# Performance work log

Hardware: AMD Instinct MI355X
Metric: run time of the kernel (lower is better)

## Reference

```python
import jax, jax.numpy as jnp
import numpy as np

B, S, D = 4, 1024, 1024
L, H, DK, DV, DFF = 2, 8, 128, 128, 2048
MASK_VALUE = -1e-30
LN_EPS = 1e-14  # K.epsilon()**2 with K.epsilon()=1e-7


def _glorot(key, shape):
    fan_in, fan_out = shape[-2], shape[-1]
    lim = np.sqrt(6.0 / (fan_in + fan_out)).astype(np.float32)
    return jax.random.uniform(key, shape, jnp.float32, -lim, lim)


def setup_inputs() -> dict:
    key = jax.random.key(0)
    ks = jax.random.split(key, 8)
    return {
        "x": jax.random.normal(ks[0], (B, S, D), jnp.float32),
        "mask": jnp.ones((B, S), jnp.float32),
        "Wq": _glorot(ks[1], (L, H, D, DK)),
        "Wk": _glorot(ks[2], (L, H, D, DK)),
        "Wv": _glorot(ks[3], (L, H, D, DV)),
        "Wo": _glorot(ks[4], (L, H * DV, D)),
        "W1": _glorot(ks[5], (L, D, DFF)),
        "b1": jnp.zeros((L, DFF), jnp.float32),
        "W2": _glorot(ks[6], (L, DFF, D)),
        "b2": jnp.zeros((L, D), jnp.float32),
        "gamma": jnp.ones((2 * L,), jnp.float32),
        "beta": jnp.zeros((2 * L,), jnp.float32),
    }


def _layernorm(x, g, b):
    mean = jnp.mean(x, axis=-1, keepdims=True)
    var = jnp.mean(jnp.square(x - mean), axis=-1, keepdims=True)
    return (x - mean) / jnp.sqrt(var + LN_EPS) * g + b


def reference(x, mask, Wq, Wk, Wv, Wo, W1, b1, W2, b2, gamma, beta):
    m = mask[:, None, None, :]  # [B,1,1,S] broadcast over heads and query positions
    num_layers = Wq.shape[0]
    for i in range(num_layers):
        # All heads at once (faithful to the per-head loop: identical math)
        q = jnp.einsum("bsd,hdk->bhsk", x, Wq[i])
        k = jnp.einsum("bsd,hdk->bhsk", x, Wk[i])
        v = jnp.einsum("bsd,hdv->bhsv", x, Wv[i])
        A = jnp.einsum("bhsk,bhtk->bhst", q, k)  # NOTE: no 1/sqrt(dk) scaling in original
        A = m * A + (1.0 - m) * MASK_VALUE
        A = jax.nn.softmax(A, axis=-1)
        o = jnp.einsum("bhst,bhtv->bhsv", A, v)
        conc = o.transpose(0, 2, 1, 3).reshape(x.shape[0], x.shape[1], -1)  # [B,S,H*DV]
        proj = conc @ Wo[i]
        x = _layernorm(x + proj, gamma[2 * i], beta[2 * i])
        ffn = jax.nn.relu(x @ W1[i] + b1[i]) @ W2[i] + b2[i]
        x = _layernorm(x + ffn, gamma[2 * i + 1], beta[2 * i + 1])
    return x
```

## Files before the change

### kernel.cpp

```cpp
#include <hip/hip_runtime.h>
#include <hip/hip_bf16.h>


typedef __bf16 bf16_t;
typedef bf16_t bf16x8 __attribute__((ext_vector_type(8)));
typedef bf16_t bf16x4v __attribute__((ext_vector_type(4)));
typedef float f32x4 __attribute__((ext_vector_type(4)));

#define MFMA16(a, b, c) __builtin_amdgcn_mfma_f32_16x16x32_bf16((a), (b), (c), 0, 0, 0)

__device__ __align__(256) unsigned char g_ws[(size_t)192 << 20];

#define MBOFF(x) ((size_t)(x) << 20)
#define OFF_X32 MBOFF(0)
#define OFF_XB_HI MBOFF(16)
#define OFF_XB_LO MBOFF(24)
#define OFF_QKV_HI MBOFF(32)
#define OFF_QKV_LO MBOFF(56)
#define OFF_VT_HI MBOFF(80)
#define OFF_VT_LO MBOFF(88)
#define OFF_CONC_HI MBOFF(96)
#define OFF_CONC_LO MBOFF(104)
#define OFF_TMP MBOFF(112)
#define OFF_H_HI MBOFF(128)
#define OFF_H_LO MBOFF(144)
#define OFF_WQKV_HI MBOFF(160)
#define OFF_WQKV_LO MBOFF(166)
#define OFF_WO_HI MBOFF(172)
#define OFF_WO_LO MBOFF(174)
#define OFF_W1_HI MBOFF(176)
#define OFF_W1_LO MBOFF(180)
#define OFF_W2_HI MBOFF(184)
#define OFF_W2_LO MBOFF(188)
#define OFF_TMP2 MBOFF(32)

__device__ __forceinline__ void split2(float v, bf16_t& h, bf16_t& l) {
  h = (bf16_t)v;
  l = (bf16_t)(v - (float)h);
}

__device__ __forceinline__ void gl2lds16(const bf16_t* g, bf16_t* l) {
  __builtin_amdgcn_global_load_lds(
      (const __attribute__((address_space(1))) unsigned int*)(g),
      (__attribute__((address_space(3))) unsigned int*)(l), 16, 0, 0);
}

template <int EPI>
__global__ __launch_bounds__(512) void gemm_bt(
    size_t a_hi, size_t a_lo, size_t b_hi, size_t b_lo,
    size_t c0o, size_t c1o, const float* __restrict__ bias,
    int M, int N, int Ktot, int Ksl) {
  const bf16_t* Ah = (const bf16_t*)(g_ws + a_hi);
  const bf16_t* Al = (const bf16_t*)(g_ws + a_lo);
  const bf16_t* Bh = (const bf16_t*)(g_ws + b_hi);
  const bf16_t* Bl = (const bf16_t*)(g_ws + b_lo);
  __shared__ __align__(16) bf16_t Ash[128 * 32];
  __shared__ __align__(16) bf16_t Asl[128 * 32];
  __shared__ __align__(16) bf16_t Bsh[128 * 32];
  __shared__ __align__(16) bf16_t Bsl[128 * 32];
  const int tid = threadIdx.x;
  const int wave = tid >> 6, lane = tid & 63;
  const int quad = lane >> 4, l16 = lane & 15;
  const int wm = wave & 3, wn = wave >> 2;
  const int m0 = blockIdx.y * 128, n0 = blockIdx.x * 128;
  const int z = blockIdx.z;
  const int srow = wave * 16 + (lane >> 2);
  const int scp = (lane & 3) ^ ((srow >> 1) & 3);
  const long agoff = (long)(m0 + srow) * Ktot + (long)z * Ksl + scp * 8;
  const long bgoff = (long)(n0 + srow) * Ktot + (long)z * Ksl + scp * 8;
  bf16_t* ldsA = Ash + wave * 512;
  bf16_t* ldsAl = Asl + wave * 512;
  bf16_t* ldsB = Bsh + wave * 512;
  bf16_t* ldsBl = Bsl + wave * 512;
  int aOff[2], bOff[4];
#pragma unroll
  for (int mt = 0; mt < 2; ++mt) {
    int R = wm * 32 + mt * 16 + l16;
    aOff[mt] = R * 32 + ((quad ^ ((R >> 1) & 3)) * 8);
  }
#pragma unroll
  for (int nt = 0; nt < 4; ++nt) {
    int R = wn * 64 + nt * 16 + l16;
    bOff[nt] = R * 32 + ((quad ^ ((R >> 1) & 3)) * 8);
  }
  f32x4 acc[2][4] = {};

  for (int k0 = 0; k0 < Ksl; k0 += 32) {
    gl2lds16(Ah + agoff + k0, ldsA);
    gl2lds16(Al + agoff + k0, ldsAl);
    gl2lds16(Bh + bgoff + k0, ldsB);
    gl2lds16(Bl + bgoff + k0, ldsBl);
    __syncthreads();
    bf16x8 ah[2], al[2], bhf[4], blf[4];
#pragma unroll
    for (int mt = 0; mt < 2; ++mt) {
      ah[mt] = *(const bf16x8*)(Ash + aOff[mt]);
      al[mt] = *(const bf16x8*)(Asl + aOff[mt]);
    }
#pragma unroll
    for (int nt = 0; nt < 4; ++nt) {
      bhf[nt] = *(const bf16x8*)(Bsh + bOff[nt]);
      blf[nt] = *(const bf16x8*)(Bsl + bOff[nt]);
    }
#pragma unroll
    for (int mt = 0; mt < 2; ++mt)
#pragma unroll
      for (int nt = 0; nt < 4; ++nt) {
        acc[mt][nt] = MFMA16(ah[mt], bhf[nt], acc[mt][nt]);
        acc[mt][nt] = MFMA16(ah[mt], blf[nt], acc[mt][nt]);
        acc[mt][nt] = MFMA16(al[mt], bhf[nt], acc[mt][nt]);
      }
    __syncthreads();
  }

  float* Cf = (float*)(g_ws + (z == 0 ? c0o : c1o));
  bf16_t* Ch = (bf16_t*)(g_ws + c0o);
  bf16_t* Cl = (bf16_t*)(g_ws + c1o);
#pragma unroll
  for (int mt = 0; mt < 2; ++mt) {
    const int row0 = m0 + wm * 32 + mt * 16 + quad * 4;
#pragma unroll
    for (int nt = 0; nt < 4; ++nt) {
      const int col = n0 + wn * 64 + nt * 16 + l16;
      float bv = ((EPI >= 2) && z == 0) ? bias[col] : 0.0f;
#pragma unroll
      for (int r = 0; r < 4; ++r) {
        float v = acc[mt][nt][r] + bv;
        if (EPI == 2) v = fmaxf(v, 0.0f);
        long off = (long)(row0 + r) * N + col;
        if (EPI == 0 || EPI == 3) {
          Cf[off] = v;
        } else {
          bf16_t h, l;
          split2(v, h, l);
          Ch[off] = h;
          Cl[off] = l;
        }
      }
    }
  }
}

__global__ __launch_bounds__(256) void attn_kernel(const float* __restrict__ mask) {
  const bf16_t* QKVh = (const bf16_t*)(g_ws + OFF_QKV_HI);
  const bf16_t* QKVl = (const bf16_t*)(g_ws + OFF_QKV_LO);
  const bf16_t* VTh = (const bf16_t*)(g_ws + OFF_VT_HI);
  const bf16_t* VTl = (const bf16_t*)(g_ws + OFF_VT_LO);
  bf16_t* conch = (bf16_t*)(g_ws + OFF_CONC_HI);
  bf16_t* concl = (bf16_t*)(g_ws + OFF_CONC_LO);
  __shared__ __align__(16) bf16_t Ksh[64 * 128];
  __shared__ __align__(16) bf16_t Ksl[64 * 128];
  __shared__ __align__(16) bf16_t Vsh[128 * 64];
  __shared__ __align__(16) bf16_t Vsl[128 * 64];
  __shared__ __align__(16) bf16_t Ps[4][16 * 72];
  const int tid = threadIdx.x;
  const int wave = tid >> 6, lane = tid & 63;
  const int quad = lane >> 4, l16 = lane & 15;
  const int q0 = blockIdx.x * 64;
  const int bh = blockIdx.y, b = bh >> 3, h = bh & 7;

  bf16x8 qfh[4], qfl[4];
  const long qgbase = ((long)(b * 1024) + q0 + wave * 16 + l16) * 3072 + h * 128;
#pragma unroll
  for (int ks = 0; ks < 4; ++ks) {
    qfh[ks] = *(const bf16x8*)(QKVh + qgbase + ks * 32 + quad * 8);
    qfl[ks] = *(const bf16x8*)(QKVl + qgbase + ks * 32 + quad * 8);
  }

  const int sKrow4 = wave * 16 + (lane >> 4);
  const int sVrow = wave * 32 + (lane >> 3);
  const int sVc = (lane & 7) ^ (sVrow & 7);
  const long vgbase = (long)bh * 131072 + (long)sVrow * 1024 + sVc * 8;

  f32x4 o[8] = {};
  float mi[4] = {-1e30f, -1e30f, -1e30f, -1e30f};
  float li[4] = {0.f, 0.f, 0.f, 0.f};

  for (int t0 = 0; t0 < 1024; t0 += 64) {
#pragma unroll
    for (int j = 0; j < 4; ++j) {
      const int r = sKrow4 + j * 4;
      const int c = (lane & 15) ^ ((r & 7) * 2);
      const long kg = ((long)(b * 1024) + t0 + r) * 3072 + 1024 + h * 128 + c * 8;
      gl2lds16(QKVh + kg, Ksh + (wave * 16 + j * 4) * 128);
      gl2lds16(QKVl + kg, Ksl + (wave * 16 + j * 4) * 128);
    }
#pragma unroll
    for (int j = 0; j < 4; ++j) {
      const long vg = vgbase + (long)(j * 8) * 1024 + t0;
      gl2lds16(VTh + vg, Vsh + (wave * 32 + j * 8) * 64);
      gl2lds16(VTl + vg, Vsl + (wave * 32 + j * 8) * 64);
    }
    __syncthreads();
    f32x4 s4[4] = {};
#pragma unroll
    for (int nt = 0; nt < 4; ++nt) {
      const int krow = nt * 16 + l16;
      const int ksw = (krow & 7) * 2;
#pragma unroll
      for (int ks = 0; ks < 4; ++ks) {
        const int so = krow * 128 + (((ks * 4 + quad) ^ ksw) * 8);
        bf16x8 kfh = *(const bf16x8*)(Ksh + so);
        bf16x8 kfl = *(const bf16x8*)(Ksl + so);
        s4[nt] = MFMA16(qfh[ks], kfh, s4[nt]);
        s4[nt] = MFMA16(qfh[ks], kfl, s4[nt]);
        s4[nt] = MFMA16(qfl[ks], kfh, s4[nt]);
      }
    }
#pragma unroll
    for (int nt = 0; nt < 4; ++nt) {
      float mv = mask[b * 1024 + t0 + nt * 16 + l16];
      float addv = (1.0f - mv) * (-1e-30f);
#pragma unroll
      for (int r = 0; r < 4; ++r) s4[nt][r] = mv * s4[nt][r] + addv;
    }
#pragma unroll
    for (int r = 0; r < 4; ++r) {
      float mx = fmaxf(fmaxf(s4[0][r], s4[1][r]), fmaxf(s4[2][r], s4[3][r]));
#pragma unroll
      for (int off = 1; off < 16; off <<= 1) mx = fmaxf(mx, __shfl_xor(mx, off, 64));
      float mnew = fmaxf(mi[r], mx);
      float alpha = __expf(mi[r] - mnew);
      float rs = 0.0f;
#pragma unroll
      for (int nt = 0; nt < 4; ++nt) {
        float p = __expf(s4[nt][r] - mnew);
        s4[nt][r] = p;
        rs += p;
      }
#pragma unroll
      for (int off = 1; off < 16; off <<= 1) rs += __shfl_xor(rs, off, 64);
      li[r] = li[r] * alpha + rs;
      mi[r] = mnew;
#pragma unroll
      for (int on = 0; on < 8; ++on) o[on][r] *= alpha;
    }
#pragma unroll
    for (int nt = 0; nt < 4; ++nt)
#pragma unroll
      for (int r = 0; r < 4; ++r)
        Ps[wave][(quad * 4 + r) * 72 + nt * 16 + l16] = (bf16_t)s4[nt][r];
    bf16x8 pf[2];
#pragma unroll
    for (int k2 = 0; k2 < 2; ++k2)
      pf[k2] = *(const bf16x8*)(&Ps[wave][l16 * 72 + k2 * 32 + quad * 8]);
#pragma unroll
    for (int k2 = 0; k2 < 2; ++k2) {
#pragma unroll
      for (int on = 0; on < 8; ++on) {
        const int vrow = on * 16 + l16;
        const int so = vrow * 64 + (((k2 * 4 + quad) ^ (vrow & 7)) * 8);
        bf16x8 vfh = *(const bf16x8*)(Vsh + so);
        bf16x8 vfl = *(const bf16x8*)(Vsl + so);
        o[on] = MFMA16(pf[k2], vfh, o[on]);
        o[on] = MFMA16(pf[k2], vfl, o[on]);
      }
    }
    __syncthreads();
  }
  const int srow_o = q0 + wave * 16 + quad * 4;
#pragma unroll
  for (int r = 0; r < 4; ++r) {
    float inv = 1.0f / li[r];
#pragma unroll
    for (int on = 0; on < 8; ++on) {
      float v = o[on][r] * inv;
      bf16_t hh, ll;
      split2(v, hh, ll);
      long off = (long)(b * 1024 + srow_o + r) * 1024 + h * 128 + on * 16 + l16;
      conch[off] = hh;
      concl[off] = ll;
    }
  }
}

__global__ __launch_bounds__(256) void ln_kernel(
    const float* __restrict__ gamma, const float* __restrict__ beta, int gidx,
    float* __restrict__ extf) {
  const float* xres = (const float*)(g_ws + OFF_X32);
  const float* y1 = (const float*)(g_ws + OFF_TMP);
  const float* y2 = (const float*)(g_ws + OFF_TMP2);
  float* xout = (float*)(g_ws + OFF_X32);
  bf16_t* xbh = (bf16_t*)(g_ws + OFF_XB_HI);
  bf16_t* xbl = (bf16_t*)(g_ws + OFF_XB_LO);
  const int row = blockIdx.x, tid = threadIdx.x;
  const int wave = tid >> 6, lane = tid & 63;
  const long base = (long)row * 1024 + tid * 4;
  float4 xv = *(const float4*)(xres + base);
  float4 yv = *(const float4*)(y1 + base);
  float4 y2v = *(const float4*)(y2 + base);
  float v0 = xv.x + yv.x + y2v.x, v1 = xv.y + yv.y + y2v.y;
  float v2 = xv.z + yv.z + y2v.z, v3 = xv.w + yv.w + y2v.w;
  float s1 = v0 + v1 + v2 + v3;
  float s2 = v0 * v0 + v1 * v1 + v2 * v2 + v3 * v3;
#pragma unroll
  for (int off = 1; off < 64; off <<= 1) {
    s1 += __shfl_xor(s1, off, 64);
    s2 += __shfl_xor(s2, off, 64);
  }
  __shared__ __align__(16) float r1[4], r2[4];
  if (lane == 0) { r1[wave] = s1; r2[wave] = s2; }
  __syncthreads();
  s1 = r1[0] + r1[1] + r1[2] + r1[3];
  s2 = r2[0] + r2[1] + r2[2] + r2[3];
  const float mean = s1 * (1.0f / 1024.0f);
  float var = s2 * (1.0f / 1024.0f) - mean * mean;
  var = fmaxf(var, 0.0f);
  const float inv = rsqrtf(var + 1e-14f);
  const float g = gamma[gidx], be = beta[gidx];
  float o0 = (v0 - mean) * inv * g + be;
  float o1 = (v1 - mean) * inv * g + be;
  float o2 = (v2 - mean) * inv * g + be;
  float o3 = (v3 - mean) * inv * g + be;
  float4 ov = {o0, o1, o2, o3};
  *(float4*)(xout + base) = ov;
  if (extf) {
    *(float4*)(extf + base) = ov;
  } else {
    bf16_t h0, l0, h1, l1, h2, l2, h3, l3;
    split2(o0, h0, l0); split2(o1, h1, l1);
    split2(o2, h2, l2); split2(o3, h3, l3);
    bf16x4v hv = {h0, h1, h2, h3};
    bf16x4v lv = {l0, l1, l2, l3};
    *(bf16x4v*)(xbh + base) = hv;
    *(bf16x4v*)(xbl + base) = lv;
  }
}

__global__ __launch_bounds__(256) void cast_f2b(const float* __restrict__ in) {
  float* out = (float*)(g_ws + OFF_X32);
  bf16_t* outh = (bf16_t*)(g_ws + OFF_XB_HI);
  bf16_t* outl = (bf16_t*)(g_ws + OFF_XB_LO);
  long i = ((long)blockIdx.x * 256 + threadIdx.x) * 4;
  float4 v = *(const float4*)(in + i);
  *(float4*)(out + i) = v;
  bf16_t h0, l0, h1, l1, h2, l2, h3, l3;
  split2(v.x, h0, l0); split2(v.y, h1, l1);
  split2(v.z, h2, l2); split2(v.w, h3, l3);
  bf16x4v hv = {h0, h1, h2, h3};
  bf16x4v lv = {l0, l1, l2, l3};
  *(bf16x4v*)(outh + i) = hv;
  *(bf16x4v*)(outl + i) = lv;
}

__global__ __launch_bounds__(256) void transp_split(
    const float* __restrict__ in, size_t oh_off, size_t ol_off, int R, int C) {
  bf16_t* oh = (bf16_t*)(g_ws + oh_off);
  bf16_t* ol = (bf16_t*)(g_ws + ol_off);
  __shared__ float tile[32][33];
  const int tx = threadIdx.x, ty = threadIdx.y;
  const int c0 = blockIdx.x * 32, r0 = blockIdx.y * 32;
#pragma unroll
  for (int j = 0; j < 4; ++j)
    tile[ty + j * 8][tx] = in[(long)(r0 + ty + j * 8) * C + c0 + tx];
  __syncthreads();
#pragma unroll
  for (int j = 0; j < 4; ++j) {
    float v = tile[tx][ty + j * 8];
    bf16_t h, l;
    split2(v, h, l);
    long off = (long)(c0 + ty + j * 8) * R + r0 + tx;
    oh[off] = h;
    ol[off] = l;
  }
}

__global__ __launch_bounds__(256) void qkvw_trans(
    const float* __restrict__ Wq, const float* __restrict__ Wk,
    const float* __restrict__ Wv) {
  bf16_t* oh = (bf16_t*)(g_ws + OFF_WQKV_HI);
  bf16_t* ol = (bf16_t*)(g_ws + OFF_WQKV_LO);
  __shared__ float tile[32][33];
  const int tx = threadIdx.x, ty = threadIdx.y;
  const int z = blockIdx.z, mat = z >> 3, h = z & 7;
  const float* src = (mat == 0 ? Wq : (mat == 1 ? Wk : Wv)) + h * 131072;
  const int c0 = blockIdx.x * 32, r0 = blockIdx.y * 32;
#pragma unroll
  for (int j = 0; j < 4; ++j)
    tile[ty + j * 8][tx] = src[(r0 + ty + j * 8) * 128 + c0 + tx];
  __syncthreads();
  const int nbase = mat * 1024 + h * 128;
#pragma unroll
  for (int j = 0; j < 4; ++j) {
    float v = tile[tx][ty + j * 8];
    bf16_t hh, ll;
    split2(v, hh, ll);
    long off = (long)(nbase + c0 + ty + j * 8) * 1024 + r0 + tx;
    oh[off] = hh;
    ol[off] = ll;
  }
}

__global__ __launch_bounds__(256) void vt_trans() {
  const bf16_t* QKVh = (const bf16_t*)(g_ws + OFF_QKV_HI);
  const bf16_t* QKVl = (const bf16_t*)(g_ws + OFF_QKV_LO);
  bf16_t* VTh = (bf16_t*)(g_ws + OFF_VT_HI);
  bf16_t* VTl = (bf16_t*)(g_ws + OFF_VT_LO);
  __shared__ bf16_t th[32][34];
  __shared__ bf16_t tl[32][34];
  const int tx = threadIdx.x, ty = threadIdx.y;
  const int bh = blockIdx.z, b = bh >> 3, h = bh & 7;
  const int s0 = blockIdx.x * 32, v0 = blockIdx.y * 32;
#pragma unroll
  for (int j = 0; j < 4; ++j) {
    long src = ((long)(b * 1024) + s0 + ty + j * 8) * 3072 + 2048 + h * 128 + v0 + tx;
    th[ty + j * 8][tx] = QKVh[src];
    tl[ty + j * 8][tx] = QKVl[src];
  }
  __syncthreads();
#pragma unroll
  for (int j = 0; j < 4; ++j) {
    long off = (long)bh * 131072 + (long)(v0 + ty + j * 8) * 1024 + s0 + tx;
    VTh[off] = th[tx][ty + j * 8];
    VTl[off] = tl[tx][ty + j * 8];
  }
}

extern "C" void kernel_launch(void* const* d_in, const int* in_sizes, int n_in,
                              void* d_out, int out_size, void* d_ws, size_t ws_size,
                              hipStream_t stream) {
  const float* x_in = (const float*)d_in[0];
  const float* mask = (const float*)d_in[1];
  const float* Wq = (const float*)d_in[2];
  const float* Wk = (const float*)d_in[3];
  const float* Wv = (const float*)d_in[4];
  const float* Wo = (const float*)d_in[5];
  const float* W1 = (const float*)d_in[6];
  const float* b1 = (const float*)d_in[7];
  const float* W2 = (const float*)d_in[8];
  const float* b2 = (const float*)d_in[9];
  const float* gamma = (const float*)d_in[10];
  const float* beta = (const float*)d_in[11];
  float* out = (float*)d_out;
  (void)d_ws; (void)ws_size; (void)in_sizes; (void)n_in; (void)out_size;

  const dim3 tb(32, 8);
  cast_f2b<<<4096, 256, 0, stream>>>(x_in);

  for (int l = 0; l < 2; ++l) {
    qkvw_trans<<<dim3(4, 32, 24), tb, 0, stream>>>(
        Wq + (long)l * 1048576, Wk + (long)l * 1048576, Wv + (long)l * 1048576);
    transp_split<<<dim3(32, 32), tb, 0, stream>>>(Wo + (long)l * 1048576,
                                                  OFF_WO_HI, OFF_WO_LO, 1024, 1024);
    transp_split<<<dim3(64, 32), tb, 0, stream>>>(W1 + (long)l * 2097152,
                                                  OFF_W1_HI, OFF_W1_LO, 1024, 2048);
    transp_split<<<dim3(32, 64), tb, 0, stream>>>(W2 + (long)l * 2097152,
                                                  OFF_W2_HI, OFF_W2_LO, 2048, 1024);

    gemm_bt<1><<<dim3(24, 32, 1), 512, 0, stream>>>(
        OFF_XB_HI, OFF_XB_LO, OFF_WQKV_HI, OFF_WQKV_LO,
        OFF_QKV_HI, OFF_QKV_LO, nullptr, 4096, 3072, 1024, 1024);
    vt_trans<<<dim3(32, 4, 32), tb, 0, stream>>>();
    attn_kernel<<<dim3(16, 32), 256, 0, stream>>>(mask);
    gemm_bt<0><<<dim3(8, 32, 2), 512, 0, stream>>>(
        OFF_CONC_HI, OFF_CONC_LO, OFF_WO_HI, OFF_WO_LO,
        OFF_TMP, OFF_TMP2, nullptr, 4096, 1024, 1024, 512);
    ln_kernel<<<4096, 256, 0, stream>>>(gamma, beta, 2 * l, nullptr);
    gemm_bt<2><<<dim3(16, 32, 1), 512, 0, stream>>>(
        OFF_XB_HI, OFF_XB_LO, OFF_W1_HI, OFF_W1_LO,
        OFF_H_HI, OFF_H_LO, b1 + l * 2048, 4096, 2048, 1024, 1024);
    gemm_bt<3><<<dim3(8, 32, 2), 512, 0, stream>>>(
        OFF_H_HI, OFF_H_LO, OFF_W2_HI, OFF_W2_LO,
        OFF_TMP, OFF_TMP2, b2 + l * 1024, 4096, 1024, 2048, 1024);
    ln_kernel<<<4096, 256, 0, stream>>>(gamma, beta, 2 * l + 1,
                                        (l == 1) ? out : nullptr);
  }
}
```

Baseline: 835.1 us.

## Add 256x256-tile double-buffered split-bf16 GEMM for QKV projection

```diff
diff --git a/kernel.cpp b/kernel.cpp
--- a/kernel.cpp
+++ b/kernel.cpp
@@ -43,6 +43,150 @@
   __builtin_amdgcn_global_load_lds(
       (const __attribute__((address_space(1))) unsigned int*)(g),
       (__attribute__((address_space(3))) unsigned int*)(l), 16, 0, 0);
+}
+
+template <int EPI>
+__global__ __launch_bounds__(512, 2) void gemm256(
+    size_t a_hi, size_t a_lo, size_t b_hi, size_t b_lo,
+    size_t c0o, size_t c1o, const float* __restrict__ bias,
+    int M, int N, int Ktot, int Ksl) {
+  const bf16_t* Ah = (const bf16_t*)(g_ws + a_hi);
+  const bf16_t* Al = (const bf16_t*)(g_ws + a_lo);
+  const bf16_t* Bh = (const bf16_t*)(g_ws + b_hi);
+  const bf16_t* Bl = (const bf16_t*)(g_ws + b_lo);
+  __shared__ __align__(16) bf16_t sAh[2][256 * 32];
+  __shared__ __align__(16) bf16_t sAl[2][256 * 32];
+  __shared__ __align__(16) bf16_t sBh[2][256 * 32];
+  __shared__ __align__(16) bf16_t sBl[2][256 * 32];
+  const int tid = threadIdx.x;
+  const int wave = tid >> 6, lane = tid & 63;
+  const int quad = lane >> 4, l16 = lane & 15;
+  const int wm = wave & 1, wn = wave >> 1;
+  const int m0 = blockIdx.y * 256, n0 = blockIdx.x * 256;
+  const int srow_s = lane >> 2;
+  const int scp = (lane & 3) ^ ((lane >> 3) & 3);
+  const long aoff0 = (long)(m0 + wave * 32 + srow_s) * Ktot + scp * 8;
+  const long aoff1 = aoff0 + (long)16 * Ktot;
+  const long boff0 = (long)(n0 + wave * 32 + srow_s) * Ktot + scp * 8;
+  const long boff1 = boff0 + (long)16 * Ktot;
+  const int ldsw0 = wave * 1024;
+  const int ldsw1 = wave * 1024 + 512;
+  const int fsw = quad ^ ((l16 >> 1) & 3);
+  int aOff[8], bOff[4];
+#pragma unroll
+  for (int mt = 0; mt < 8; ++mt)
+    aOff[mt] = (wm * 128 + mt * 16 + l16) * 32 + fsw * 8;
+#pragma unroll
+  for (int nt = 0; nt < 4; ++nt)
+    bOff[nt] = (wn * 64 + nt * 16 + l16) * 32 + fsw * 8;
+
+  f32x4 acc[8][4] = {};
+  const int nk = Ksl >> 5;
+
+#define STAGE_H1(bufi, ko)                      \
+  gl2lds16(Ah + aoff0 + (ko), &sAh[bufi][ldsw0]); \
+  gl2lds16(Al + aoff0 + (ko), &sAl[bufi][ldsw0]); \
+  gl2lds16(Bh + boff0 + (ko), &sBh[bufi][ldsw0]); \
+  gl2lds16(Bl + boff0 + (ko), &sBl[bufi][ldsw0]);
+#define STAGE_H2(bufi, ko)                      \
+  gl2lds16(Ah + aoff1 + (ko), &sAh[bufi][ldsw1]); \
+  gl2lds16(Al + aoff1 + (ko), &sAl[bufi][ldsw1]); \
+  gl2lds16(Bh + boff1 + (ko), &sBh[bufi][ldsw1]); \
+  gl2lds16(Bl + boff1 + (ko), &sBl[bufi][ldsw1]);
+
+  STAGE_H1(0, 0);
+  STAGE_H2(0, 0);
+
+  for (int t = 0; t < nk; ++t) {
+    const int cur = t & 1, nxt = cur ^ 1;
+    const int ko = (t + 1) * 32;
+    const bool pf = (t + 1 < nk);
+    if (pf) {
+      STAGE_H1(nxt, ko);
+      asm volatile("s_waitcnt vmcnt(4)" ::: "memory");
+    } else {
+      asm volatile("s_waitcnt vmcnt(0)" ::: "memory");
+    }
+    __builtin_amdgcn_sched_barrier(0);
+    __builtin_amdgcn_s_barrier();
+    __builtin_amdgcn_sched_barrier(0);
+    bf16x8 bh4[4], bl4[4], ah2[4], al2[4];
+#pragma unroll
+    for (int nt = 0; nt < 4; ++nt) {
+      bh4[nt] = *(const bf16x8*)(&sBh[cur][bOff[nt]]);
+      bl4[nt] = *(const bf16x8*)(&sBl[cur][bOff[nt]]);
+    }
+#pragma unroll
+    for (int mt = 0; mt < 4; ++mt) {
+      ah2[mt] = *(const bf16x8*)(&sAh[cur][aOff[mt]]);
+      al2[mt] = *(const bf16x8*)(&sAl[cur][aOff[mt]]);
+    }
+    asm volatile("s_waitcnt lgkmcnt(0)" ::: "memory");
+    __builtin_amdgcn_sched_barrier(0);
+    __builtin_amdgcn_s_setprio(1);
+#pragma unroll
+    for (int mt = 0; mt < 4; ++mt)
+#pragma unroll
+      for (int nt = 0; nt < 4; ++nt) {
+        acc[mt][nt] = MFMA16(ah2[mt], bh4[nt], acc[mt][nt]);
+        acc[mt][nt] = MFMA16(ah2[mt], bl4[nt], acc[mt][nt]);
+        acc[mt][nt] = MFMA16(al2[mt], bh4[nt], acc[mt][nt]);
+      }
+    __builtin_amdgcn_s_setprio(0);
+    __builtin_amdgcn_sched_barrier(0);
+    __builtin_amdgcn_s_barrier();
+    if (pf) {
+      STAGE_H2(nxt, ko);
+    }
+#pragma unroll
+    for (int mt = 0; mt < 4; ++mt) {
+      ah2[mt] = *(const bf16x8*)(&sAh[cur][aOff[mt + 4]]);
+      al2[mt] = *(const bf16x8*)(&sAl[cur][aOff[mt + 4]]);
+    }
+    asm volatile("s_waitcnt lgkmcnt(0)" ::: "memory");
+    __builtin_amdgcn_sched_barrier(0);
+    __builtin_amdgcn_s_setprio(1);
+#pragma unroll
+    for (int mt = 0; mt < 4; ++mt)
+#pragma unroll
+      for (int nt = 0; nt < 4; ++nt) {
+        acc[mt + 4][nt] = MFMA16(ah2[mt], bh4[nt], acc[mt + 4][nt]);
+        acc[mt + 4][nt] = MFMA16(ah2[mt], bl4[nt], acc[mt + 4][nt]);
+        acc[mt + 4][nt] = MFMA16(al2[mt], bh4[nt], acc[mt + 4][nt]);
+      }
+    __builtin_amdgcn_s_setprio(0);
+    __builtin_amdgcn_sched_barrier(0);
+    __builtin_amdgcn_s_barrier();
+  }
+#undef STAGE_H1
+#undef STAGE_H2
+
+  float* Cf = (float*)(g_ws + c0o);
+  bf16_t* Ch = (bf16_t*)(g_ws + c0o);
+  bf16_t* Cl = (bf16_t*)(g_ws + c1o);
+#pragma unroll
+  for (int mt = 0; mt < 8; ++mt) {
+    const int row0 = m0 + wm * 128 + mt * 16 + quad * 4;
+#pragma unroll
+    for (int nt = 0; nt < 4; ++nt) {
+      const int col = n0 + wn * 64 + nt * 16 + l16;
+      float bv = (EPI >= 2) ? bias[col] : 0.0f;
+#pragma unroll
+      for (int r = 0; r < 4; ++r) {
+        float v = acc[mt][nt][r] + bv;
+        if (EPI == 2) v = fmaxf(v, 0.0f);
+        long off = (long)(row0 + r) * N + col;
+        if (EPI == 0 || EPI == 3) {
+          Cf[off] = v;
+        } else {
+          bf16_t h, l;
+          split2(v, h, l);
+          Ch[off] = h;
+          Cl[off] = l;
+        }
+      }
+    }
+  }
 }
 
 template <int EPI>
@@ -447,7 +591,7 @@
     transp_split<<<dim3(32, 64), tb, 0, stream>>>(W2 + (long)l * 2097152,
                                                   OFF_W2_HI, OFF_W2_LO, 2048, 1024);
 
-    gemm_bt<1><<<dim3(24, 32, 1), 512, 0, stream>>>(
+    gemm256<1><<<dim3(12, 16, 1), 512, 0, stream>>>(
         OFF_XB_HI, OFF_XB_LO, OFF_WQKV_HI, OFF_WQKV_LO,
         OFF_QKV_HI, OFF_QKV_LO, nullptr, 4096, 3072, 1024, 1024);
     vt_trans<<<dim3(32, 4, 32), tb, 0, stream>>>();
```

Result: no change. 848.2 us (+1.6%).

## Double-buffer LDS tiles in split-bf16 GEMM to overlap global loads with MFMA

Applied to the files above, without the earlier changes.

```diff
diff --git a/kernel.cpp b/kernel.cpp
--- a/kernel.cpp
+++ b/kernel.cpp
@@ -54,10 +54,10 @@
   const bf16_t* Al = (const bf16_t*)(g_ws + a_lo);
   const bf16_t* Bh = (const bf16_t*)(g_ws + b_hi);
   const bf16_t* Bl = (const bf16_t*)(g_ws + b_lo);
-  __shared__ __align__(16) bf16_t Ash[128 * 32];
-  __shared__ __align__(16) bf16_t Asl[128 * 32];
-  __shared__ __align__(16) bf16_t Bsh[128 * 32];
-  __shared__ __align__(16) bf16_t Bsl[128 * 32];
+  __shared__ __align__(16) bf16_t Ash[2][128 * 32];
+  __shared__ __align__(16) bf16_t Asl[2][128 * 32];
+  __shared__ __align__(16) bf16_t Bsh[2][128 * 32];
+  __shared__ __align__(16) bf16_t Bsl[2][128 * 32];
   const int tid = threadIdx.x;
   const int wave = tid >> 6, lane = tid & 63;
   const int quad = lane >> 4, l16 = lane & 15;
@@ -68,10 +68,7 @@
   const int scp = (lane & 3) ^ ((srow >> 1) & 3);
   const long agoff = (long)(m0 + srow) * Ktot + (long)z * Ksl + scp * 8;
   const long bgoff = (long)(n0 + srow) * Ktot + (long)z * Ksl + scp * 8;
-  bf16_t* ldsA = Ash + wave * 512;
-  bf16_t* ldsAl = Asl + wave * 512;
-  bf16_t* ldsB = Bsh + wave * 512;
-  bf16_t* ldsBl = Bsl + wave * 512;
+  const int ldsw = wave * 512;
   int aOff[2], bOff[4];
 #pragma unroll
   for (int mt = 0; mt < 2; ++mt) {
@@ -84,23 +81,37 @@
     bOff[nt] = R * 32 + ((quad ^ ((R >> 1) & 3)) * 8);
   }
   f32x4 acc[2][4] = {};
-
-  for (int k0 = 0; k0 < Ksl; k0 += 32) {
-    gl2lds16(Ah + agoff + k0, ldsA);
-    gl2lds16(Al + agoff + k0, ldsAl);
-    gl2lds16(Bh + bgoff + k0, ldsB);
-    gl2lds16(Bl + bgoff + k0, ldsBl);
-    __syncthreads();
+  const int nk = Ksl >> 5;
+
+  gl2lds16(Ah + agoff, &Ash[0][ldsw]);
+  gl2lds16(Al + agoff, &Asl[0][ldsw]);
+  gl2lds16(Bh + bgoff, &Bsh[0][ldsw]);
+  gl2lds16(Bl + bgoff, &Bsl[0][ldsw]);
+
+  for (int t = 0; t < nk; ++t) {
+    const int cur = t & 1, nxt = cur ^ 1;
+    const long ko = (long)(t + 1) * 32;
+    if (t + 1 < nk) {
+      gl2lds16(Ah + agoff + ko, &Ash[nxt][ldsw]);
+      gl2lds16(Al + agoff + ko, &Asl[nxt][ldsw]);
+      gl2lds16(Bh + bgoff + ko, &Bsh[nxt][ldsw]);
+      gl2lds16(Bl + bgoff + ko, &Bsl[nxt][ldsw]);
+      asm volatile("s_waitcnt vmcnt(4)" ::: "memory");
+    } else {
+      asm volatile("s_waitcnt vmcnt(0)" ::: "memory");
+    }
+    __builtin_amdgcn_s_barrier();
+    __builtin_amdgcn_sched_barrier(0);
     bf16x8 ah[2], al[2], bhf[4], blf[4];
 #pragma unroll
     for (int mt = 0; mt < 2; ++mt) {
-      ah[mt] = *(const bf16x8*)(Ash + aOff[mt]);
-      al[mt] = *(const bf16x8*)(Asl + aOff[mt]);
+      ah[mt] = *(const bf16x8*)(&Ash[cur][aOff[mt]]);
+      al[mt] = *(const bf16x8*)(&Asl[cur][aOff[mt]]);
     }
 #pragma unroll
     for (int nt = 0; nt < 4; ++nt) {
-      bhf[nt] = *(const bf16x8*)(Bsh + bOff[nt]);
-      blf[nt] = *(const bf16x8*)(Bsl + bOff[nt]);
+      bhf[nt] = *(const bf16x8*)(&Bsh[cur][bOff[nt]]);
+      blf[nt] = *(const bf16x8*)(&Bsl[cur][bOff[nt]]);
     }
 #pragma unroll
     for (int mt = 0; mt < 2; ++mt)
@@ -110,7 +121,8 @@
         acc[mt][nt] = MFMA16(ah[mt], blf[nt], acc[mt][nt]);
         acc[mt][nt] = MFMA16(al[mt], bhf[nt], acc[mt][nt]);
       }
-    __syncthreads();
+    asm volatile("s_waitcnt lgkmcnt(0)" ::: "memory");
+    __builtin_amdgcn_s_barrier();
   }
 
   float* Cf = (float*)(g_ws + (z == 0 ? c0o : c1o));
```

Result: no change. 827.4 us (-0.9%).
